# Optimization experiments

Measured on AMD Instinct MI355X. Metric: run time of the kernel, lower is better.

Reference implementation:

```python
import jax, jax.numpy as jnp
import numpy as np

B, T, D, H = 32, 512, 1024, 16
HD = D // H  # 64


def setup_inputs() -> dict:
    key = jax.random.key(0)
    ks = jax.random.split(key, 12)
    s_in = 1.0 / np.sqrt(D)
    x = jax.random.normal(ks[0], (B, T, D), dtype=jnp.float32)
    Wi = jax.random.normal(ks[1], (D, D), dtype=jnp.float32) * s_in
    bi = jnp.zeros((D,), dtype=jnp.float32)
    Wk = jax.random.normal(ks[2], (H, D, HD), dtype=jnp.float32) * s_in
    bk = jnp.zeros((H, HD), dtype=jnp.float32)
    Wq = jax.random.normal(ks[3], (H, D, HD), dtype=jnp.float32) * s_in
    bq = jnp.zeros((H, HD), dtype=jnp.float32)
    Wv = jax.random.normal(ks[4], (H, D, HD), dtype=jnp.float32) * s_in
    bv = jnp.zeros((H, HD), dtype=jnp.float32)
    Wo = jax.random.normal(ks[5], (D, D), dtype=jnp.float32) * s_in
    bo = jnp.zeros((D,), dtype=jnp.float32)
    return {"x": x, "Wi": Wi, "bi": bi, "Wk": Wk, "bk": bk,
            "Wq": Wq, "bq": bq, "Wv": Wv, "bv": bv, "Wo": Wo, "bo": bo}


def reference(x, Wi, bi, Wk, bk, Wq, bq, Wv, bv, Wo, bo):
    # in_proj
    h = x @ Wi + bi  # [B,T,D]
    # per-head K/Q/V projections, vectorized over heads
    k = jnp.einsum('btd,hde->bhte', h, Wk) + bk[None, :, None, :]  # [B,H,T,HD]
    q = jnp.einsum('btd,hde->bhte', h, Wq) + bq[None, :, None, :]
    v = jnp.einsum('btd,hde->bhte', h, Wv) + bv[None, :, None, :]
    # NOTE: original computes wei = k @ q^T (keys as rows), masks with tril,
    # softmax over last axis (queries). Faithfully reproduced (no scaling).
    wei = jnp.einsum('bhtd,bhsd->bhts', k, q)  # [B,H,T,T]
    causal = jnp.tril(jnp.ones((T, T), dtype=bool))
    wei = jnp.where(causal, wei, -jnp.inf)
    wei = jax.nn.softmax(wei, axis=-1)
    # dropout: eval mode (identity)
    out = jnp.einsum('bhts,bhsd->bhtd', wei, v)  # [B,H,T,HD]
    out = out.transpose(0, 2, 1, 3).reshape(B, T, D)  # concat heads on last dim
    return out @ Wo + bo
```

## Files before the change

kernel.cpp:

```cpp
#include <hip/hip_runtime.h>
#include <hip/hip_bf16.h>
#include <stdint.h>

#define NTOK 16384

typedef _Float16 f16;
typedef f16   f16x8 __attribute__((ext_vector_type(8)));
typedef float f32x4 __attribute__((ext_vector_type(4)));

__device__ __forceinline__ float bf2f(ushort h){
  union { uint32_t u; float f; } v; v.u = ((uint32_t)h) << 16; return v.f;
}
__device__ __forceinline__ ushort f2bf(float f){
  union { float f; uint32_t u; } v; v.f = f;
  uint32_t u = v.u;
  return (ushort)((u + 0x7FFFu + ((u >> 16) & 1u)) >> 16);
}
__device__ __forceinline__ ushort f2h(float f){
  return __builtin_bit_cast(ushort, (f16)f);
}
__device__ __forceinline__ f16x8 ld16(const ushort* p){
  uint4 u = *(const uint4*)p;
  return __builtin_bit_cast(f16x8, u);
}
__device__ __forceinline__ float ldf(const void* p, size_t idx, int isf32){
  if (isf32) return ((const float*)p)[idx];
  return bf2f(((const ushort*)p)[idx]);
}

__device__ __forceinline__ const ushort* swz(const ushort* base, uint row, uint chunk){
  return base + (size_t)row*64u + (size_t)((chunk ^ (row & 7u))*8u);
}

__device__ __forceinline__ void stage64(const ushort* g, uint strideEl,
                                        ushort* ldsbase, uint tid){
  uint w = tid >> 6;
  #pragma unroll
  for (int i = 0; i < 2; ++i){
    uint lc  = i*256u + tid;
    uint row = lc >> 3, cp = lc & 7u;
    uint c   = cp ^ (row & 7u);
    const ushort* gp = g + (size_t)row*strideEl + c*8u;
    ushort* lp = ldsbase + (size_t)(i*256u + w*64u)*8u;
    __builtin_amdgcn_global_load_lds((const __attribute__((address_space(1))) void*)gp,
        (__attribute__((address_space(3))) void*)lp, 16, 0, 0);
  }
}

__global__ __launch_bounds__(256) void kdetect(const uint* __restrict__ wi, int* __restrict__ flag){
  __shared__ int cnt;
  if (threadIdx.x == 0) cnt = 0;
  __syncthreads();
  uint w = wi[threadIdx.x];
  uint e = (w >> 7) & 0xFFu;
  if (e >= 100u && e <= 130u) atomicAdd(&cnt, 1);
  __syncthreads();
  if (threadIdx.x == 0) flag[0] = (cnt < 128) ? 1 : 0;
}

__global__ __launch_bounds__(256) void kbias(const void* bi, const void* bo,
                                             const void* bk, const void* bq, const void* bv,
                                             const int* __restrict__ flag,
                                             float* bi_f, float* bo_f, float* bqkv_f){
  int f = flag[0];
  uint id = blockIdx.x*256u + threadIdx.x;
  if (id < 1024u)       bi_f[id]         = ldf(bi, id, f);
  else if (id < 2048u)  bo_f[id - 1024u] = ldf(bo, id - 1024u, f);
  else {
    uint j = id - 2048u;
    uint sel = j >> 10, i = j & 1023u;
    const void* src = (sel == 0) ? bk : ((sel == 1) ? bq : bv);
    bqkv_f[j] = ldf(src, i, f);
  }
}

__global__ __launch_bounds__(256) void ktranspose(const void* __restrict__ in,
                                                  const int* __restrict__ flag,
                                                  ushort* __restrict__ out){
  __shared__ float tile[64][65];
  int f = flag[0];
  uint R0 = blockIdx.x*64u, C0 = blockIdx.y*64u, t = threadIdx.x;
  #pragma unroll
  for (int i = 0; i < 16; ++i){
    uint id = i*256u + t, r = id >> 6, c = id & 63u;
    tile[r][c] = ldf(in, (size_t)(R0 + r)*1024u + C0 + c, f);
  }
  __syncthreads();
  #pragma unroll
  for (int i = 0; i < 16; ++i){
    uint id = i*256u + t, r = id >> 6, c = id & 63u;
    out[(size_t)(C0 + r)*1024u + R0 + c] = f2h(tile[c][r]);
  }
}

__global__ __launch_bounds__(256) void kqkvpack(const void* Wk, const void* Wq, const void* Wv,
                                                const int* __restrict__ flag,
                                                ushort* __restrict__ WqkvT){
  __shared__ float tile[64][65];
  int f = flag[0];
  uint sh = blockIdx.x;
  uint sel = sh >> 4, h = sh & 15u;
  uint D0 = blockIdx.y*64u, t = threadIdx.x;
  const void* W = (sel == 0) ? Wk : ((sel == 1) ? Wq : Wv);
  #pragma unroll
  for (int i = 0; i < 16; ++i){
    uint id = i*256u + t, r = id >> 6, c = id & 63u;
    tile[r][c] = ldf(W, (size_t)h*65536u + (size_t)(D0 + r)*64u + c, f);
  }
  __syncthreads();
  #pragma unroll
  for (int i = 0; i < 16; ++i){
    uint id = i*256u + t, r = id >> 6, c = id & 63u;
    WqkvT[(size_t)(sel*1024u + h*64u + r)*1024u + D0 + c] = f2h(tile[c][r]);
  }
}

__global__ __launch_bounds__(256) void kcvt_x(const void* __restrict__ x,
                                              const int* __restrict__ flag,
                                              ushort* __restrict__ xh){
  int f = flag[0];
  size_t g = (size_t)(blockIdx.x*256u + threadIdx.x)*8u;
  ushort o[8];
  if (f){
    const float4* xf = (const float4*)((const float*)x + g);
    float4 a = xf[0], b = xf[1];
    o[0] = f2h(a.x); o[1] = f2h(a.y); o[2] = f2h(a.z); o[3] = f2h(a.w);
    o[4] = f2h(b.x); o[5] = f2h(b.y); o[6] = f2h(b.z); o[7] = f2h(b.w);
  } else {
    uint4 u = *(const uint4*)((const ushort*)x + g);
    ushort s[8];
    *(uint4*)s = u;
    #pragma unroll
    for (int i = 0; i < 8; ++i) o[i] = f2h(bf2f(s[i]));
  }
  *(uint4*)(xh + g) = *(uint4*)o;
}

template<int MODE>
__global__ __launch_bounds__(256, 4) void kgemm(const ushort* __restrict__ A, const ushort* __restrict__ Bt,
                                                const float* __restrict__ bias, void* __restrict__ Cv,
                                                ushort* __restrict__ Vt, const int* __restrict__ dtf,
                                                int M, int N, int K){
  __shared__ ushort sA[128*32];
  __shared__ ushort sB[128*32];
  uint tid = threadIdx.x, w = tid >> 6, lane = tid & 63u, quad = lane >> 4, l15 = lane & 15u;
  uint bm = blockIdx.x, bn = blockIdx.y;
  uint wm = w >> 1, wn = w & 1u;
  f32x4 acc[4][4] = {};

  for (int k0 = 0; k0 < K; k0 += 32){
    #pragma unroll
    for (int i = 0; i < 2; ++i){
      uint c   = (w*2u + i)*64u + lane;
      uint row = c >> 2, ko = (c & 3u)*8u;
      const ushort* gA = A  + (size_t)(bm*128u + row)*K + k0 + ko;
      const ushort* gB = Bt + (size_t)(bn*128u + row)*K + k0 + ko;
      __builtin_amdgcn_global_load_lds((const __attribute__((address_space(1))) void*)gA,
          (__attribute__((address_space(3))) void*)(sA + (w*2u + i)*512u), 16, 0, 0);
      __builtin_amdgcn_global_load_lds((const __attribute__((address_space(1))) void*)gB,
          (__attribute__((address_space(3))) void*)(sB + (w*2u + i)*512u), 16, 0, 0);
    }
    __syncthreads();
    f16x8 aF[4], bF[4];
    #pragma unroll
    for (int i = 0; i < 4; ++i) aF[i] = *(const f16x8*)(sA + (wm*64u + i*16u + l15)*32u + quad*8u);
    #pragma unroll
    for (int j = 0; j < 4; ++j) bF[j] = *(const f16x8*)(sB + (wn*64u + j*16u + l15)*32u + quad*8u);
    #pragma unroll
    for (int i = 0; i < 4; ++i)
      #pragma unroll
      for (int j = 0; j < 4; ++j)
        acc[i][j] = __builtin_amdgcn_mfma_f32_16x16x32_f16(aF[i], bF[j], acc[i][j], 0, 0, 0);
    __syncthreads();
  }
  int f32out = (MODE == 2) ? dtf[0] : 0;
  const float L2E = 1.44269504088896340736f;
  #pragma unroll
  for (int j = 0; j < 4; ++j){
    uint col = bn*128u + wn*64u + j*16u + l15;
    float bj = bias[col];
    #pragma unroll
    for (int i = 0; i < 4; ++i){
      uint row0 = bm*128u + wm*64u + i*16u + quad*4u;
      #pragma unroll
      for (int r = 0; r < 4; ++r){
        float val = acc[i][j][r] + bj;
        uint row = row0 + r;
        if (MODE == 0){
          ((ushort*)Cv)[(size_t)row*N + col] = f2h(val);
        } else if (MODE == 1){
          if (col < 2048u){
            float v2 = (col >= 1024u) ? val * L2E : val;
            ((ushort*)Cv)[(size_t)row*2048u + col] = f2h(v2);
          } else {
            uint c2 = col - 2048u;
            Vt[(size_t)(((row >> 9)*16u + (c2 >> 6))*64u + (c2 & 63u))*512u + (row & 511u)] = f2h(val);
          }
        } else {
          if (f32out) ((float*)Cv)[(size_t)row*N + col] = val;
          else        ((ushort*)Cv)[(size_t)row*N + col] = f2bf(val);
        }
      }
    }
  }
}

__global__ __launch_bounds__(256, 4) void kattn(const ushort* __restrict__ kq,
                                                const ushort* __restrict__ Vt,
                                                ushort* __restrict__ Out){
  __shared__ ushort sQ[2][64*64];
  __shared__ ushort sV[2][64*64];
  __shared__ ushort pbuf[4][16*64];
  uint tid = threadIdx.x, w = tid >> 6, lane = tid & 63u, quad = lane >> 4, l15 = lane & 15u;
  uint bh = blockIdx.x, tt = 7u - blockIdx.y;
  uint b = bh >> 4, h = bh & 15u;
  uint t0 = tt*64u;
  const float MNEG = -1.0e30f;

  stage64(kq + (size_t)(b*512u + t0)*2048u + h*64u, 2048u, (ushort*)pbuf, tid);
  stage64(kq + (size_t)(b*512u)*2048u + 1024u + h*64u, 2048u, sQ[0], tid);
  stage64(Vt + (size_t)(bh*64u)*512u, 512u, sV[0], tid);
  __syncthreads();

  f16x8 aK[2];
  aK[0] = ld16(swz((const ushort*)pbuf, w*16u + l15, quad));
  aK[1] = ld16(swz((const ushort*)pbuf, w*16u + l15, 4u + quad));

  float m[4], l[4];
  f32x4 oacc[4];
  #pragma unroll
  for (int r = 0; r < 4; ++r){ m[r] = MNEG; l[r] = 0.f; }
  #pragma unroll
  for (int je = 0; je < 4; ++je) oacc[je] = (f32x4){0.f, 0.f, 0.f, 0.f};

  ushort* pw = (ushort*)pbuf + w*1024u;

  for (uint st = 0; st <= tt; ++st){
    uint cur = st & 1u;
    if (st) __syncthreads();
    if (st < tt){
      uint s1 = (st + 1u)*64u;
      stage64(kq + (size_t)(b*512u + s1)*2048u + 1024u + h*64u, 2048u, sQ[1u - cur], tid);
      stage64(Vt + (size_t)(bh*64u)*512u + s1, 512u, sV[1u - cur], tid);
    }
    f32x4 sacc[4];
    #pragma unroll
    for (int j = 0; j < 4; ++j){
      f16x8 bq0 = ld16(swz(sQ[cur], j*16u + l15, quad));
      f16x8 bq1 = ld16(swz(sQ[cur], j*16u + l15, 4u + quad));
      f32x4 s = (f32x4){0.f, 0.f, 0.f, 0.f};
      s = __builtin_amdgcn_mfma_f32_16x16x32_f16(aK[0], bq0, s, 0, 0, 0);
      s = __builtin_amdgcn_mfma_f32_16x16x32_f16(aK[1], bq1, s, 0, 0, 0);
      sacc[j] = s;
    }
    if (st == tt){
      #pragma unroll
      for (int j = 0; j < 4; ++j)
        #pragma unroll
        for (int r = 0; r < 4; ++r)
          if (j*16u + l15 > w*16u + quad*4u + (uint)r) sacc[j][r] = MNEG;
    }
    float alpha[4];
    #pragma unroll
    for (int r = 0; r < 4; ++r){
      float v = fmaxf(fmaxf(sacc[0][r], sacc[1][r]), fmaxf(sacc[2][r], sacc[3][r]));
      v = fmaxf(v, __shfl_xor(v, 1));
      v = fmaxf(v, __shfl_xor(v, 2));
      v = fmaxf(v, __shfl_xor(v, 4));
      v = fmaxf(v, __shfl_xor(v, 8));
      float mn = fmaxf(m[r], v);
      alpha[r] = exp2f(m[r] - mn);
      m[r] = mn;
    }
    #pragma unroll
    for (int j = 0; j < 4; ++j)
      #pragma unroll
      for (int r = 0; r < 4; ++r)
        sacc[j][r] = exp2f(sacc[j][r] - m[r]);
    #pragma unroll
    for (int r = 0; r < 4; ++r){
      float s = sacc[0][r] + sacc[1][r] + sacc[2][r] + sacc[3][r];
      s += __shfl_xor(s, 1);
      s += __shfl_xor(s, 2);
      s += __shfl_xor(s, 4);
      s += __shfl_xor(s, 8);
      l[r] = l[r]*alpha[r] + s;
    }
    #pragma unroll
    for (int je = 0; je < 4; ++je)
      #pragma unroll
      for (int r = 0; r < 4; ++r)
        oacc[je][r] *= alpha[r];
    #pragma unroll
    for (int j = 0; j < 4; ++j)
      #pragma unroll
      for (int r = 0; r < 4; ++r){
        uint t = quad*4u + (uint)r;
        pw[t*64u + (((j*2u + (l15 >> 3)) ^ (t & 7u))*8u) + (l15 & 7u)] = f2h(sacc[j][r]);
      }
    f16x8 aP0 = ld16(swz(pw, l15, quad));
    f16x8 aP1 = ld16(swz(pw, l15, 4u + quad));
    #pragma unroll
    for (int je = 0; je < 4; ++je){
      f16x8 bv0 = ld16(swz(sV[cur], je*16u + l15, quad));
      f16x8 bv1 = ld16(swz(sV[cur], je*16u + l15, 4u + quad));
      oacc[je] = __builtin_amdgcn_mfma_f32_16x16x32_f16(aP0, bv0, oacc[je], 0, 0, 0);
      oacc[je] = __builtin_amdgcn_mfma_f32_16x16x32_f16(aP1, bv1, oacc[je], 0, 0, 0);
    }
  }
  float inv[4];
  #pragma unroll
  for (int r = 0; r < 4; ++r) inv[r] = 1.0f / l[r];
  #pragma unroll
  for (int je = 0; je < 4; ++je){
    uint e = h*64u + je*16u + l15;
    #pragma unroll
    for (int r = 0; r < 4; ++r){
      uint t = t0 + w*16u + quad*4u + (uint)r;
      Out[(size_t)(b*512u + t)*1024u + e] = f2h(oacc[je][r]*inv[r]);
    }
  }
}


extern "C" void kernel_launch(void* const* d_in, const int* in_sizes, int n_in,
                              void* d_out, int out_size, void* d_ws, size_t ws_size,
                              hipStream_t stream){
  const void* x  = d_in[0];
  const void* Wi = d_in[1];
  const void* bi = d_in[2];
  const void* Wk = d_in[3];
  const void* bk = d_in[4];
  const void* Wq = d_in[5];
  const void* bq = d_in[6];
  const void* Wv = d_in[7];
  const void* bv = d_in[8];
  const void* Wo = d_in[9];
  const void* bo = d_in[10];
  char* ws = (char*)d_ws;

  const size_t MB = 1u << 20;
  int*    flag   = (int*)ws;
  float*  bi_f   = (float*)(ws + 4096);
  float*  bo_f   = (float*)(ws + 8192);
  float*  bqkv_f = (float*)(ws + 12288);
  ushort* WiT    = (ushort*)(ws + 32768);
  ushort* WoT    = (ushort*)(ws + 32768 + 2*MB);
  ushort* WqkvT  = (ushort*)(ws + 32768 + 4*MB);
  ushort* xh     = (ushort*)(ws + 32768 + 10*MB);
  ushort* kq     = (ushort*)(ws + 32768 + 10*MB);
  ushort* hbuf   = (ushort*)(ws + 32768 + 74*MB);
  ushort* Vt     = (ushort*)(ws + 32768 + 106*MB);

  kdetect<<<dim3(1), dim3(256), 0, stream>>>((const uint*)Wi, flag);
  kbias<<<dim3(20), dim3(256), 0, stream>>>(bi, bo, bk, bq, bv, flag, bi_f, bo_f, bqkv_f);
  ktranspose<<<dim3(16, 16), dim3(256), 0, stream>>>(Wi, flag, WiT);
  ktranspose<<<dim3(16, 16), dim3(256), 0, stream>>>(Wo, flag, WoT);
  kqkvpack<<<dim3(48, 16), dim3(256), 0, stream>>>(Wk, Wq, Wv, flag, WqkvT);
  kcvt_x<<<dim3(8192), dim3(256), 0, stream>>>(x, flag, xh);

  kgemm<0><<<dim3(128, 8),  dim3(256), 0, stream>>>(xh,   WiT,   bi_f,   hbuf, nullptr, nullptr, NTOK, 1024, 1024);
  kgemm<1><<<dim3(128, 24), dim3(256), 0, stream>>>(hbuf, WqkvT, bqkv_f, kq,   Vt,      nullptr, NTOK, 3072, 1024);
  kattn<<<dim3(512, 8), dim3(256), 0, stream>>>(kq, Vt, hbuf);
  kgemm<2><<<dim3(128, 8),  dim3(256), 0, stream>>>(hbuf, WoT,   bo_f,   d_out, nullptr, flag,   NTOK, 1024, 1024);
}
```

Measured before the change: 502.8 us.

## Double GEMM K-tile to 64 with swizzled LDS and split QKV GEMM

The GEMM kernel now stages 64-wide K slices into XOR-swizzled LDS tiles and runs two MFMA sub-steps per barrier pair. This halves the number of synchronisations and is meant to cut LDS bank conflicts on fragment reads. The fused QKV GEMM is split into two launches, one writing K/Q and one writing the transposed V, which removes the per-element branch in the epilogue. In exchange, LDS per block doubles, which may reduce occupancy, and the extra launch reads hbuf a second time.

```diff
diff --git a/kernel.cpp b/kernel.cpp
--- a/kernel.cpp
+++ b/kernel.cpp
@@ -41,6 +41,21 @@
     uint row = lc >> 3, cp = lc & 7u;
     uint c   = cp ^ (row & 7u);
     const ushort* gp = g + (size_t)row*strideEl + c*8u;
+    ushort* lp = ldsbase + (size_t)(i*256u + w*64u)*8u;
+    __builtin_amdgcn_global_load_lds((const __attribute__((address_space(1))) void*)gp,
+        (__attribute__((address_space(3))) void*)lp, 16, 0, 0);
+  }
+}
+
+__device__ __forceinline__ void stage128(const ushort* g, int K,
+                                         ushort* ldsbase, uint tid){
+  uint w = tid >> 6;
+  #pragma unroll
+  for (int i = 0; i < 4; ++i){
+    uint lc  = i*256u + tid;
+    uint row = lc >> 3, cp = lc & 7u;
+    uint c   = cp ^ (row & 7u);
+    const ushort* gp = g + (size_t)row*(size_t)K + c*8u;
     ushort* lp = ldsbase + (size_t)(i*256u + w*64u)*8u;
     __builtin_amdgcn_global_load_lds((const __attribute__((address_space(1))) void*)gp,
         (__attribute__((address_space(3))) void*)lp, 16, 0, 0);
@@ -141,36 +156,30 @@
                                                 const float* __restrict__ bias, void* __restrict__ Cv,
                                                 ushort* __restrict__ Vt, const int* __restrict__ dtf,
                                                 int M, int N, int K){
-  __shared__ ushort sA[128*32];
-  __shared__ ushort sB[128*32];
+  __shared__ ushort sA[128*64];
+  __shared__ ushort sB[128*64];
   uint tid = threadIdx.x, w = tid >> 6, lane = tid & 63u, quad = lane >> 4, l15 = lane & 15u;
   uint bm = blockIdx.x, bn = blockIdx.y;
   uint wm = w >> 1, wn = w & 1u;
   f32x4 acc[4][4] = {};
 
-  for (int k0 = 0; k0 < K; k0 += 32){
-    #pragma unroll
-    for (int i = 0; i < 2; ++i){
-      uint c   = (w*2u + i)*64u + lane;
-      uint row = c >> 2, ko = (c & 3u)*8u;
-      const ushort* gA = A  + (size_t)(bm*128u + row)*K + k0 + ko;
-      const ushort* gB = Bt + (size_t)(bn*128u + row)*K + k0 + ko;
-      __builtin_amdgcn_global_load_lds((const __attribute__((address_space(1))) void*)gA,
-          (__attribute__((address_space(3))) void*)(sA + (w*2u + i)*512u), 16, 0, 0);
-      __builtin_amdgcn_global_load_lds((const __attribute__((address_space(1))) void*)gB,
-          (__attribute__((address_space(3))) void*)(sB + (w*2u + i)*512u), 16, 0, 0);
-    }
+  for (int k0 = 0; k0 < K; k0 += 64){
+    stage128(A  + (size_t)(bm*128u)*(size_t)K + k0, K, sA, tid);
+    stage128(Bt + (size_t)(bn*128u)*(size_t)K + k0, K, sB, tid);
     __syncthreads();
-    f16x8 aF[4], bF[4];
-    #pragma unroll
-    for (int i = 0; i < 4; ++i) aF[i] = *(const f16x8*)(sA + (wm*64u + i*16u + l15)*32u + quad*8u);
-    #pragma unroll
-    for (int j = 0; j < 4; ++j) bF[j] = *(const f16x8*)(sB + (wn*64u + j*16u + l15)*32u + quad*8u);
-    #pragma unroll
-    for (int i = 0; i < 4; ++i)
-      #pragma unroll
-      for (int j = 0; j < 4; ++j)
-        acc[i][j] = __builtin_amdgcn_mfma_f32_16x16x32_f16(aF[i], bF[j], acc[i][j], 0, 0, 0);
+    #pragma unroll
+    for (int kk = 0; kk < 2; ++kk){
+      f16x8 aF[4], bF[4];
+      #pragma unroll
+      for (int i = 0; i < 4; ++i) aF[i] = ld16(swz(sA, wm*64u + (uint)i*16u + l15, (uint)kk*4u + quad));
+      #pragma unroll
+      for (int j = 0; j < 4; ++j) bF[j] = ld16(swz(sB, wn*64u + (uint)j*16u + l15, (uint)kk*4u + quad));
+      #pragma unroll
+      for (int i = 0; i < 4; ++i)
+        #pragma unroll
+        for (int j = 0; j < 4; ++j)
+          acc[i][j] = __builtin_amdgcn_mfma_f32_16x16x32_f16(aF[i], bF[j], acc[i][j], 0, 0, 0);
+    }
     __syncthreads();
   }
   int f32out = (MODE == 2) ? dtf[0] : 0;
@@ -188,14 +197,11 @@
         uint row = row0 + r;
         if (MODE == 0){
           ((ushort*)Cv)[(size_t)row*N + col] = f2h(val);
-        } else if (MODE == 1){
-          if (col < 2048u){
-            float v2 = (col >= 1024u) ? val * L2E : val;
-            ((ushort*)Cv)[(size_t)row*2048u + col] = f2h(v2);
-          } else {
-            uint c2 = col - 2048u;
-            Vt[(size_t)(((row >> 9)*16u + (c2 >> 6))*64u + (c2 & 63u))*512u + (row & 511u)] = f2h(val);
-          }
+        } else if (MODE == 3){
+          float v2 = (col >= 1024u) ? val * L2E : val;
+          ((ushort*)Cv)[(size_t)row*2048u + col] = f2h(v2);
+        } else if (MODE == 4){
+          Vt[(size_t)(((row >> 9)*16u + (col >> 6))*64u + (col & 63u))*512u + (row & 511u)] = f2h(val);
         } else {
           if (f32out) ((float*)Cv)[(size_t)row*N + col] = val;
           else        ((ushort*)Cv)[(size_t)row*N + col] = f2bf(val);
@@ -359,8 +365,9 @@
   kqkvpack<<<dim3(48, 16), dim3(256), 0, stream>>>(Wk, Wq, Wv, flag, WqkvT);
   kcvt_x<<<dim3(8192), dim3(256), 0, stream>>>(x, flag, xh);
 
-  kgemm<0><<<dim3(128, 8),  dim3(256), 0, stream>>>(xh,   WiT,   bi_f,   hbuf, nullptr, nullptr, NTOK, 1024, 1024);
-  kgemm<1><<<dim3(128, 24), dim3(256), 0, stream>>>(hbuf, WqkvT, bqkv_f, kq,   Vt,      nullptr, NTOK, 3072, 1024);
+  kgemm<0><<<dim3(128, 8),  dim3(256), 0, stream>>>(xh,   WiT,           bi_f,          hbuf, nullptr, nullptr, NTOK, 1024, 1024);
+  kgemm<3><<<dim3(128, 16), dim3(256), 0, stream>>>(hbuf, WqkvT,         bqkv_f,        kq,   nullptr, nullptr, NTOK, 2048, 1024);
+  kgemm<4><<<dim3(128, 8),  dim3(256), 0, stream>>>(hbuf, WqkvT + (size_t)2048*1024, bqkv_f + 2048, nullptr, Vt, nullptr, NTOK, 1024, 1024);
   kattn<<<dim3(512, 8), dim3(256), 0, stream>>>(kq, Vt, hbuf);
-  kgemm<2><<<dim3(128, 8),  dim3(256), 0, stream>>>(hbuf, WoT,   bo_f,   d_out, nullptr, flag,   NTOK, 1024, 1024);
-}
+  kgemm<2><<<dim3(128, 8),  dim3(256), 0, stream>>>(hbuf, WoT,           bo_f,          d_out, nullptr, flag,   NTOK, 1024, 1024);
+}
```

Result: faster. 452.0 us (-10.1%).
